# Kernel optimization log

Measured on AMD Instinct MI355X. Metric: run time of the kernel, lower is better.

Reference implementation:

```python
import jax, jax.numpy as jnp
import numpy as np

N = 512
NQ = 8
SIGMA = 1.0
NORM_FACTOR = 90.4756
NC = NORM_FACTOR / (2.0 * np.pi)  # norm_const = norm_factor / twopi


def make_kernels(r, sigma, nc):
    # Gaussian-screened Coulomb kernel g(r) = erf(a r)/r, a = 1/(sigma*sqrt(2)),
    # and its Cartesian tensor derivatives D1..D4 (D_n = (1/r d/dr)^n g).
    n = r.shape[0]
    d = r[None, :, :] - r[:, None, :]          # d[i,j] = r_j - r_i  [n,n,3]
    eye = jnp.eye(n, dtype=bool)
    r2 = jnp.sum(d * d, axis=-1)
    rr = jnp.sqrt(jnp.where(eye, 1.0, r2))     # safe diagonal
    a = 1.0 / (sigma * np.sqrt(2.0))
    a2 = a * a
    E = jax.scipy.special.erf(a * rr)
    G = (2.0 * a / np.sqrt(np.pi)) * jnp.exp(-a2 * rr * rr)
    ir = 1.0 / rr
    ir2 = ir * ir; ir3 = ir2 * ir; ir4 = ir2 * ir2; ir5 = ir4 * ir
    ir6 = ir4 * ir2; ir7 = ir6 * ir; ir8 = ir4 * ir4; ir9 = ir8 * ir
    off = jnp.where(eye, 0.0, 1.0).astype(r.dtype)  # remove self interaction
    g  = E * ir * off
    D1 = (G * ir2 - E * ir3) * off
    D2 = (3.0 * E * ir5 - 3.0 * G * ir4 - 2.0 * a2 * G * ir2) * off
    D3 = (-15.0 * E * ir7 + 15.0 * G * ir6 + 10.0 * a2 * G * ir4
          + 4.0 * a2 * a2 * G * ir2) * off
    D4 = (105.0 * E * ir9 - 105.0 * G * ir8 - 70.0 * a2 * G * ir6
          - 28.0 * a2 * a2 * G * ir4 - 8.0 * a2 * a2 * a2 * G * ir2) * off
    I3 = jnp.eye(3, dtype=r.dtype)
    f_qq = nc * g                                        # [n,n]
    f_qu = -nc * D1[..., None] * d                       # [n,n,3]
    dd = d[..., :, None] * d[..., None, :]               # [n,n,3,3]
    f_uu = nc * (D2[..., None, None] * dd + D1[..., None, None] * I3)
    ddd = dd[..., None] * d[..., None, None, :]          # [n,n,3,3,3]
    s3 = (jnp.einsum('ab,ijc->ijabc', I3, d)
          + jnp.einsum('ac,ijb->ijabc', I3, d)
          + jnp.einsum('bc,ija->ijabc', I3, d))
    f_Qu = nc * (D3[..., None, None, None] * ddd + D2[..., None, None, None] * s3)
    dddd = ddd[..., None] * d[:, :, None, None, None, :]  # [n,n,3,3,3,3]
    s6 = (jnp.einsum('ab,ijcd->ijabcd', I3, dd)
          + jnp.einsum('ac,ijbd->ijabcd', I3, dd)
          + jnp.einsum('ad,ijbc->ijabcd', I3, dd)
          + jnp.einsum('bc,ijad->ijabcd', I3, dd)
          + jnp.einsum('bd,ijac->ijabcd', I3, dd)
          + jnp.einsum('cd,ijab->ijabcd', I3, dd))
    iso = (jnp.einsum('ab,cd->abcd', I3, I3)
           + jnp.einsum('ac,bd->abcd', I3, I3)
           + jnp.einsum('ad,bc->abcd', I3, I3))
    f_QQ = nc * (D4[..., None, None, None, None] * dddd
                 + D3[..., None, None, None, None] * s6
                 + D2[..., None, None, None, None] * iso)
    return f_qq, f_qu, f_uu, f_Qu, f_QQ


def ewald_realspace(q, r, u, quad, kappa, alpha):
    f_qq, f_qu, f_uu, f_Qu, f_QQ = make_kernels(r, SIGMA, NC)
    # charge-charge
    e_phi = jnp.einsum('iq,ij->jq', q, f_qq)
    pot = 0.5 * jnp.einsum('iq,iq->q', e_phi, q)
    # charge-dipole
    e_phi_u = jnp.einsum('iqc,ijc->jq', u, f_qu)
    e_phi = e_phi + e_phi_u
    pot = pot + jnp.einsum('iq,iq->q', e_phi_u, q)
    # dipole-dipole
    E_u = jnp.einsum('ijcd,iqc->jqd', f_uu, u)
    pot = pot - 0.5 * jnp.einsum('iqc,iqc->q', u, E_u)
    # quadrupole terms
    e_phi_Q = 0.5 * jnp.einsum('iqab,ijab->jq', quad, f_uu)
    E_Q = -0.5 * jnp.einsum('iqab,ijabc->jqc', quad, f_Qu)
    e_phi = e_phi + e_phi_Q
    pot = pot + jnp.einsum('iq,iq->q', q, e_phi_Q)
    QQ = jnp.einsum('ijabcd,jqcd->iqab', f_QQ, quad)
    pot = pot + 0.125 * jnp.einsum('iqab,iqab->q', quad, QQ)
    pot = pot - jnp.einsum('iqc,iqc->q', u, E_Q)
    # induced charges (kappa)
    q_induced = -kappa * e_phi
    pot = pot + 0.5 * jnp.sum(e_phi * q_induced, axis=0)
    # field and induced dipoles (alpha, scalar polarizability)
    e_field = jnp.einsum('iq,ijc->jqc', q, f_qu) + E_u + E_Q
    u_induced = e_field * alpha[..., None]
    pot = pot - 0.5 * jnp.sum(e_field * u_induced, axis=(0, 2))
    return pot.sum().reshape(-1), q_induced, u_induced


def setup_inputs():
    key = jax.random.key(0)
    ks = jax.random.split(key, 6)
    r = jax.random.normal(ks[0], (N, 3), jnp.float32) * 5.0
    q = jax.random.normal(ks[1], (N, NQ), jnp.float32)
    u = jax.random.normal(ks[2], (N, NQ, 3), jnp.float32)
    quad = jax.random.normal(ks[3], (N, NQ, 3, 3), jnp.float32)
    kappa = jax.random.uniform(ks[4], (N, NQ), jnp.float32)
    alpha = jax.random.uniform(ks[5], (N, NQ), jnp.float32)
    cell = jnp.zeros((1, 3, 3), jnp.float32)   # det < 1e-6 -> realspace branch
    batch = jnp.zeros((N,), jnp.int32)         # single system
    return {'q': q, 'r': r, 'cell': cell, 'batch': batch, 'u': u,
            'quad': quad, 'kappa': kappa, 'alpha': alpha}


def reference(q, r, cell, batch, u, quad, kappa, alpha):
    # cell is zero (det < 1e-6) and batch is a single graph -> realspace path
    return ewald_realspace(q, r, u, quad, kappa, alpha)
```

## Files before the change

### kernel.cpp

```cpp
#include <hip/hip_runtime.h>
#include <math.h>

#define NA 512
#define NQC 8

#define NCf ((float)(90.4756 / 6.28318530717958647692))
#define A_ERF 0.70710678118654752f
#define G_COEF 0.79788456080286536f

__global__ __launch_bounds__(512)
void main_kernel(const float* __restrict__ qarr,
                 const float* __restrict__ rarr,
                 const float* __restrict__ uarr,
                 const float* __restrict__ quadarr,
                 const float* __restrict__ kaparr,
                 const float* __restrict__ alparr,
                 float* __restrict__ out,
                 float* __restrict__ potpart) {
    const int j    = blockIdx.x;
    const int tid  = threadIdx.x;
    const int qch  = tid & 7;
    const int lane = tid & 63;
    const int wv   = tid >> 6;

    const float rjx = rarr[j*3+0], rjy = rarr[j*3+1], rjz = rarr[j*3+2];

    const int jq = j * NQC + qch;
    const float* Qj = quadarr + (size_t)jq * 9;
    const float jxx = Qj[0], jyy = Qj[4], jzz = Qj[8];
    const float jxy = 0.5f*(Qj[1]+Qj[3]);
    const float jxz = 0.5f*(Qj[2]+Qj[6]);
    const float jyz = 0.5f*(Qj[5]+Qj[7]);
    const float jtq = jxx + jyy + jzz;

    float mc0, mc1, mc2, mc3, mc4, mdx, mdy, mdz;
    {
        const int myi = ((lane >> 3) << 6) + (wv << 3) + (lane & 7);
        mdx = rjx - rarr[myi*3+0];
        mdy = rjy - rarr[myi*3+1];
        mdz = rjz - rarr[myi*3+2];
        float r2 = mdx*mdx + mdy*mdy + mdz*mdz;
        const bool diag = (myi == j);
        if (diag) r2 = 1.0f;
        const float ir  = rsqrtf(r2);
        const float rr  = r2 * ir;
        const float x   = A_ERF * rr;
        const float E2  = __expf(-0.5f * r2);
        const float G   = G_COEF * E2;
        const float t   = __builtin_amdgcn_rcpf(fmaf(0.3275911f, x, 1.0f));
        const float pol = t*(0.254829592f + t*(-0.284496736f + t*(1.421413741f
                         + t*(-1.453152027f + t*1.061405429f))));
        const float E   = fmaf(-pol, E2, 1.0f);
        const float ir2 = ir * ir;
        const float ir4 = ir2 * ir2;
        const float g   = E * ir;
        const float GmG = G - g;
        const float nco = diag ? 0.0f : NCf;
        mc0 = nco * g;
        mc1 = nco * ir2 * GmG;
        mc2 = nco * ir2 * (-3.0f*ir2*GmG - G);
        mc3 = nco * ir2 * (15.0f*ir4*GmG + 5.0f*G*ir2 + G);
        mc4 = nco * ir2 * (-105.0f*ir4*ir2*GmG - 35.0f*G*ir4 - 7.0f*G*ir2 - G);
    }

    float e0 = 0.f, eph = 0.f;
    float Fx = 0.f, Fy = 0.f, Fz = 0.f;
    float Hx = 0.f, Hy = 0.f, Hz = 0.f;
    float pQQ = 0.f;

    #pragma unroll 2
    for (int k = 0; k < 8; ++k) {
        const int iq  = k * 512 + tid;
        const int src = (k << 3) + (lane >> 3);

        const float c0 = __shfl(mc0, src, 64);
        const float c1 = __shfl(mc1, src, 64);
        const float c2 = __shfl(mc2, src, 64);
        const float c3 = __shfl(mc3, src, 64);
        const float c4 = __shfl(mc4, src, 64);
        const float dx = __shfl(mdx, src, 64);
        const float dy = __shfl(mdy, src, 64);
        const float dz = __shfl(mdz, src, 64);

        const float qi = qarr[iq];
        const float ux = uarr[iq*3+0], uy = uarr[iq*3+1], uz = uarr[iq*3+2];
        const float* Qi = quadarr + (size_t)iq * 9;
        const float xx = Qi[0], yy = Qi[4], zz = Qi[8];
        const float xy = 0.5f*(Qi[1]+Qi[3]);
        const float xz = 0.5f*(Qi[2]+Qi[6]);
        const float yz = 0.5f*(Qi[5]+Qi[7]);
        const float tqi = xx + yy + zz;

        const float ud  = ux*dx + uy*dy + uz*dz;
        const float Pdx = xx*dx + xy*dy + xz*dz;
        const float Pdy = xy*dx + yy*dy + yz*dz;
        const float Pdz = xz*dx + yz*dy + zz*dz;
        const float Pdd = Pdx*dx + Pdy*dy + Pdz*dz;

        const float t0 = c0 * qi;
        e0  += t0;
        eph += t0 - c1*ud + 0.5f*(c2*Pdd + c1*tqi);

        const float cH = 0.5f*(c2*(ud - tqi) - c3*Pdd);
        const float cF = cH + 0.5f*c2*ud - c1*qi;
        const float c1h = 0.5f * c1;
        Fx += cF*dx + c1*ux - c2*Pdx;
        Fy += cF*dy + c1*uy - c2*Pdy;
        Fz += cF*dz + c1*uz - c2*Pdz;
        Hx += cH*dx + c1h*ux - c2*Pdx;
        Hy += cH*dy + c1h*uy - c2*Pdy;
        Hz += cH*dz + c1h*uz - c2*Pdz;

        const float Rdx = jxx*dx + jxy*dy + jxz*dz;
        const float Rdy = jxy*dx + jyy*dy + jyz*dz;
        const float Rdz = jxz*dx + jyz*dy + jzz*dz;
        const float Rdd = Rdx*dx + Rdy*dy + Rdz*dz;
        const float dPR = Pdx*Rdx + Pdy*Rdy + Pdz*Rdz;
        const float frob = xx*jxx + yy*jyy + zz*jzz + 2.0f*(xy*jxy + xz*jxz + yz*jyz);
        pQQ += c4*(Pdd*Rdd)
             + c3*(jtq*Pdd + tqi*Rdd + 4.0f*dPR)
             + c2*(tqi*jtq + 2.0f*frob);
    }

    float acc[9] = {e0, eph, Fx, Fy, Fz, Hx, Hy, Hz, pQQ};
    #pragma unroll
    for (int off = 8; off < 64; off <<= 1) {
        #pragma unroll
        for (int c = 0; c < 9; ++c) acc[c] += __shfl_xor(acc[c], off, 64);
    }
    __shared__ float red[8][8][9];
    if ((lane & 56) == 0) {
        #pragma unroll
        for (int c = 0; c < 9; ++c) red[wv][lane][c] = acc[c];
    }
    __syncthreads();
    if (tid < 8) {
        float v[9];
        #pragma unroll
        for (int c = 0; c < 9; ++c) {
            float s = 0.f;
            #pragma unroll
            for (int w = 0; w < 8; ++w) s += red[w][tid][c];
            v[c] = s;
        }
        const float te0 = v[0], teph = v[1];
        const float tFx = v[2], tFy = v[3], tFz = v[4];
        const float tHx = v[5], tHy = v[6], tHz = v[7];
        const float tQQ = v[8] * 0.125f;
        const int myjq = j * NQC + tid;
        const float qj  = qarr[myjq];
        const float ujx = uarr[myjq*3+0], ujy = uarr[myjq*3+1], ujz = uarr[myjq*3+2];
        const float kapv = kaparr[myjq];
        const float alpv = alparr[myjq];

        float pot = qj * (teph - 0.5f*te0)
                  - (ujx*tHx + ujy*tHy + ujz*tHz)
                  + tQQ
                  - 0.5f * kapv * teph * teph
                  - 0.5f * alpv * (tFx*tFx + tFy*tFy + tFz*tFz);

        out[1 + myjq] = -kapv * teph;
        out[1 + NA*NQC + myjq*3 + 0] = alpv * tFx;
        out[1 + NA*NQC + myjq*3 + 1] = alpv * tFy;
        out[1 + NA*NQC + myjq*3 + 2] = alpv * tFz;

        #pragma unroll
        for (int off = 4; off; off >>= 1) pot += __shfl_xor(pot, off, 8);
        if (tid == 0) potpart[j] = pot;
    }
}

__global__ void pot_kernel(const float* __restrict__ potpart, float* __restrict__ out) {
    const int tid = threadIdx.x;
    float p = potpart[tid];
    #pragma unroll
    for (int off = 32; off; off >>= 1) p += __shfl_xor(p, off, 64);
    __shared__ float l[8];
    if ((tid & 63) == 0) l[tid >> 6] = p;
    __syncthreads();
    if (tid == 0) {
        float s = 0.f;
        #pragma unroll
        for (int w = 0; w < 8; ++w) s += l[w];
        out[0] = s;
    }
}

extern "C" void kernel_launch(void* const* d_in, const int* in_sizes, int n_in,
                              void* d_out, int out_size, void* d_ws, size_t ws_size,
                              hipStream_t stream) {
    const float* q    = (const float*)d_in[0];
    const float* r    = (const float*)d_in[1];
    const float* u    = (const float*)d_in[4];
    const float* quad = (const float*)d_in[5];
    const float* kap  = (const float*)d_in[6];
    const float* alp  = (const float*)d_in[7];
    float* out = (float*)d_out;
    float* potpart = (float*)d_ws;
    (void)ws_size; (void)in_sizes; (void)n_in; (void)out_size;

    main_kernel<<<NA, 512, 0, stream>>>(q, r, u, quad, kap, alp, out, potpart);
    pot_kernel<<<1, 512, 0, stream>>>(potpart, out);
}
```

Before: 17.77 us.

## Stage quadrupole and dipole tiles through double-buffered LDS with coalesced loads

```diff
diff --git a/kernel.cpp b/kernel.cpp
--- a/kernel.cpp
+++ b/kernel.cpp
@@ -22,6 +22,9 @@
     const int qch  = tid & 7;
     const int lane = tid & 63;
     const int wv   = tid >> 6;
+
+    __shared__ float sQ[2][NA * 9];
+    __shared__ float sU[2][NA * 3];
 
     const float rjx = rarr[j*3+0], rjy = rarr[j*3+1], rjz = rarr[j*3+2];
 
@@ -63,6 +66,16 @@
         mc4 = nco * ir2 * (-105.0f*ir4*ir2*GmG - 35.0f*G*ir4 - 7.0f*G*ir2 - G);
     }
 
+    {
+        const float* srcQ = quadarr;
+        #pragma unroll
+        for (int m = 0; m < 9; ++m) sQ[0][tid + m*512] = srcQ[tid + m*512];
+        const float* srcU = uarr;
+        #pragma unroll
+        for (int m = 0; m < 3; ++m) sU[0][tid + m*512] = srcU[tid + m*512];
+    }
+    __syncthreads();
+
     float e0 = 0.f, eph = 0.f;
     float Fx = 0.f, Fy = 0.f, Fz = 0.f;
     float Hx = 0.f, Hy = 0.f, Hz = 0.f;
@@ -70,6 +83,17 @@
 
     #pragma unroll 2
     for (int k = 0; k < 8; ++k) {
+        const int cur = k & 1, nxt = cur ^ 1;
+
+        if (k < 7) {
+            const float* srcQ = quadarr + (size_t)(k+1) * (NA * 9);
+            #pragma unroll
+            for (int m = 0; m < 9; ++m) sQ[nxt][tid + m*512] = srcQ[tid + m*512];
+            const float* srcU = uarr + (size_t)(k+1) * (NA * 3);
+            #pragma unroll
+            for (int m = 0; m < 3; ++m) sU[nxt][tid + m*512] = srcU[tid + m*512];
+        }
+
         const int iq  = k * 512 + tid;
         const int src = (k << 3) + (lane >> 3);
 
@@ -83,12 +107,15 @@
         const float dz = __shfl(mdz, src, 64);
 
         const float qi = qarr[iq];
-        const float ux = uarr[iq*3+0], uy = uarr[iq*3+1], uz = uarr[iq*3+2];
-        const float* Qi = quadarr + (size_t)iq * 9;
-        const float xx = Qi[0], yy = Qi[4], zz = Qi[8];
-        const float xy = 0.5f*(Qi[1]+Qi[3]);
-        const float xz = 0.5f*(Qi[2]+Qi[6]);
-        const float yz = 0.5f*(Qi[5]+Qi[7]);
+        const float ux = sU[cur][tid*3+0];
+        const float uy = sU[cur][tid*3+1];
+        const float uz = sU[cur][tid*3+2];
+        const float xx = sQ[cur][tid*9+0];
+        const float yy = sQ[cur][tid*9+4];
+        const float zz = sQ[cur][tid*9+8];
+        const float xy = 0.5f*(sQ[cur][tid*9+1] + sQ[cur][tid*9+3]);
+        const float xz = 0.5f*(sQ[cur][tid*9+2] + sQ[cur][tid*9+6]);
+        const float yz = 0.5f*(sQ[cur][tid*9+5] + sQ[cur][tid*9+7]);
         const float tqi = xx + yy + zz;
 
         const float ud  = ux*dx + uy*dy + uz*dz;
@@ -120,6 +147,8 @@
         pQQ += c4*(Pdd*Rdd)
              + c3*(jtq*Pdd + tqi*Rdd + 4.0f*dPR)
              + c2*(tqi*jtq + 2.0f*frob);
+
+        __syncthreads();
     }
 
     float acc[9] = {e0, eph, Fx, Fy, Fz, Hx, Hy, Hz, pQQ};
```

After: 21.05 us. 18.4% more time.
